# Optimization experiments

Measured on AMD Instinct MI355X. Metric: run time of the kernel, lower is better.

The kernel has to match this reference:

```python
import jax, jax.numpy as jnp
import numpy as np

N_E = 1024
E_DIM = 64


def setup_inputs() -> dict:
    key = jax.random.key(0)
    k_z, k_emb = jax.random.split(key)
    z = jax.random.normal(k_z, (8, 16, 32, 32, E_DIM), dtype=jnp.float32)
    embeddings = jax.random.normal(k_emb, (N_E, E_DIM), dtype=jnp.float32) * 0.02
    return {"z": z, "embeddings": embeddings}


def reference(z, embeddings):
    # flatten all leading dims: [B*T*H*W, e_dim]
    zf = z.reshape(-1, z.shape[-1])
    # squared L2 distance: ||z||^2 + ||e||^2 - 2 z.e  -> [tokens, n_e]
    d = (jnp.sum(zf ** 2, axis=1, keepdims=True)
         + jnp.sum(embeddings ** 2, axis=1)[None, :]
         - 2.0 * jnp.einsum('bd,nd->bn', zf, embeddings))
    idx = jnp.argmin(d, axis=1)
    z_q = embeddings[idx].reshape(z.shape)
    idx = idx.reshape(z.shape[:-1])
    return z_q, idx
```

## Files before the change

kernel.cpp:

```cpp
#include <hip/hip_runtime.h>

typedef short short8 __attribute__((ext_vector_type(8)));
typedef float f32x4 __attribute__((ext_vector_type(4)));

#define NTOK (8 * 16 * 32 * 32)
#define NE 1024
#define ED 64
#define TPB 256
#define MBLK 256
#define NMF 4
#define WKEY (1 << 18)
#define SCALE (-131072.0f)

__device__ __forceinline__ unsigned short bf16_rtne(float f) {
    unsigned u = __float_as_uint(f);
    return (unsigned short)((u + 0x7FFFu + ((u >> 16) & 1u)) >> 16);
}
__device__ __forceinline__ float bf16_to_f32(unsigned short h) {
    return __uint_as_float(((unsigned)h) << 16);
}

__device__ float exact_dist(const float* __restrict__ z, const float* __restrict__ emb,
                            int t, int e) {
    const float* zt = z + (size_t)t * ED;
    const float* ep = emb + (size_t)e * ED;
    float r0 = 0.f, r1 = 0.f, r2 = 0.f, r3 = 0.f;
    float r4 = 0.f, r5 = 0.f, r6 = 0.f, r7 = 0.f;
    for (int d = 0; d < ED; d += 8) {
        r0 += zt[d + 0] * zt[d + 0];
        r1 += zt[d + 1] * zt[d + 1];
        r2 += zt[d + 2] * zt[d + 2];
        r3 += zt[d + 3] * zt[d + 3];
        r4 += zt[d + 4] * zt[d + 4];
        r5 += zt[d + 5] * zt[d + 5];
        r6 += zt[d + 6] * zt[d + 6];
        r7 += zt[d + 7] * zt[d + 7];
    }
    float s1 = ((r0 + r1) + (r2 + r3)) + ((r4 + r5) + (r6 + r7));
    float q0 = 0.f, q1 = 0.f, q2 = 0.f, q3 = 0.f;
    float q4 = 0.f, q5 = 0.f, q6 = 0.f, q7 = 0.f;
    for (int d = 0; d < ED; d += 8) {
        float v0 = ep[d + 0], v1 = ep[d + 1], v2 = ep[d + 2], v3 = ep[d + 3];
        float v4 = ep[d + 4], v5 = ep[d + 5], v6 = ep[d + 6], v7 = ep[d + 7];
        q0 += v0 * v0; q1 += v1 * v1; q2 += v2 * v2; q3 += v3 * v3;
        q4 += v4 * v4; q5 += v5 * v5; q6 += v6 * v6; q7 += v7 * v7;
    }
    float s2 = ((q0 + q1) + (q2 + q3)) + ((q4 + q5) + (q6 + q7));
    float a0 = 0.f, a1 = 0.f, a2 = 0.f, a3 = 0.f;
    for (int d = 0; d < ED; d += 4) {
        a0 = fmaf(zt[d + 0], ep[d + 0], a0);
        a1 = fmaf(zt[d + 1], ep[d + 1], a1);
        a2 = fmaf(zt[d + 2], ep[d + 2], a2);
        a3 = fmaf(zt[d + 3], ep[d + 3], a3);
    }
    float g = (a0 + a1) + (a2 + a3);
    return (s1 + s2) - 2.0f * g;
}

__global__ __launch_bounds__(128) void vq_prep(
    const float* __restrict__ emb,
    unsigned short* __restrict__ bfH,
    unsigned short* __restrict__ bfL,
    float* __restrict__ s2s)
{
    const int f = blockIdx.x * 128 + threadIdx.x;
    const int col = f & 15;
    const int quad = (f >> 4) & 3;
    const int kb = (f >> 6) & 1;
    const int nt = f >> 7;
    const int e = nt * 16 + col;
    const int k0 = kb * 32 + quad * 8;

    const float* p = emb + (size_t)e * ED + k0;
    float4 v0 = *(const float4*)p;
    float4 v1 = *(const float4*)(p + 4);
    float vs[8] = {v0.x, v0.y, v0.z, v0.w, v1.x, v1.y, v1.z, v1.w};
    short8 h, l;
#pragma unroll
    for (int j = 0; j < 8; ++j) {
        float x = vs[j] * SCALE;
        unsigned short hb = bf16_rtne(x);
        float hf = bf16_to_f32(hb);
        unsigned short lb = bf16_rtne(x - hf);
        h[j] = (short)hb;
        l[j] = (short)lb;
    }
    *(short8*)&bfH[(size_t)f * 8] = h;
    *(short8*)&bfL[(size_t)f * 8] = l;

    if (f < 4096) {
        const int row = f >> 2;
        const float4* rp = (const float4*)(emb + (size_t)row * ED + (f & 3) * 16);
        float4 a = rp[0], b = rp[1], c = rp[2], d = rp[3];
        float s = a.x * a.x + a.y * a.y + a.z * a.z + a.w * a.w
                + b.x * b.x + b.y * b.y + b.z * b.z + b.w * b.w
                + c.x * c.x + c.y * c.y + c.z * c.z + c.w * c.w
                + d.x * d.x + d.y * d.y + d.z * d.z + d.w * d.w;
        s += __shfl_xor(s, 1);
        s += __shfl_xor(s, 2);
        if ((f & 3) == 0) s2s[row] = s * 65536.0f;
    }
}

__global__ void __launch_bounds__(TPB) vq_main(
    const float* __restrict__ z,
    const float* __restrict__ emb,
    const unsigned short* __restrict__ bfH,
    const unsigned short* __restrict__ bfL,
    const float* __restrict__ s2s_g,
    float* __restrict__ zq_out,
    float* __restrict__ idx_out)
{
    __shared__ float s2L[NE];
    __shared__ int idx_lds[MBLK];

    const int tid = threadIdx.x;
    const int lane = tid & 63;
    const int wv = __builtin_amdgcn_readfirstlane(tid >> 6);
    const int col = lane & 15;
    const int quad = lane >> 4;
    const int blockTok = blockIdx.x * MBLK;

    for (int i = tid; i < NE; i += TPB) s2L[i] = s2s_g[i];

    short8 Ah[NMF][2], Al[NMF][2];
#pragma unroll
    for (int mf = 0; mf < NMF; ++mf) {
#pragma unroll
        for (int kf = 0; kf < 2; ++kf) {
            const float* zp = z + (size_t)(blockTok + wv * 64 + mf * 16 + col) * ED
                              + kf * 32 + quad * 8;
            float4 v0 = *(const float4*)zp;
            float4 v1 = *(const float4*)(zp + 4);
            float vs[8] = {v0.x, v0.y, v0.z, v0.w, v1.x, v1.y, v1.z, v1.w};
            short8 h, l;
#pragma unroll
            for (int j = 0; j < 8; ++j) {
                float x = vs[j];
                unsigned short hb = bf16_rtne(x);
                float hf = bf16_to_f32(hb);
                unsigned short lb = bf16_rtne(x - hf);
                h[j] = (short)hb;
                l[j] = (short)lb;
            }
            Ah[mf][kf] = h;
            Al[mf][kf] = l;
        }
    }

    int aK[NMF][4], bK[NMF][4];
#pragma unroll
    for (int mf = 0; mf < NMF; ++mf)
#pragma unroll
        for (int r = 0; r < 4; ++r) { aK[mf][r] = 0x7FFFFFFF; bK[mf][r] = 0x7FFFFFFF; }

    const uint4* u4H = (const uint4*)bfH;
    const uint4* u4L = (const uint4*)bfL;

    uint4 cB0 = u4H[lane];
    uint4 cB1 = u4H[64 + lane];
    uint4 cB2 = u4L[lane];
    uint4 cB3 = u4L[64 + lane];

    __syncthreads();

    for (int nt = 0; nt < 64; ++nt) {
        const int nb = (((nt + 1) & 63) << 7) + lane;
        uint4 nB0 = u4H[nb];
        uint4 nB1 = u4H[nb + 64];
        uint4 nB2 = u4L[nb];
        uint4 nB3 = u4L[nb + 64];

        short8 Bh0 = __builtin_bit_cast(short8, cB0);
        short8 Bh1 = __builtin_bit_cast(short8, cB1);
        short8 Bl0 = __builtin_bit_cast(short8, cB2);
        short8 Bl1 = __builtin_bit_cast(short8, cB3);

        const float s2v = s2L[nt * 16 + col];
        const int e = nt * 16 + col;
#pragma unroll
        for (int mf = 0; mf < NMF; ++mf) {
            f32x4 cc = {s2v, s2v, s2v, s2v};
            cc = __builtin_amdgcn_mfma_f32_16x16x32_bf16(Ah[mf][0], Bh0, cc, 0, 0, 0);
            cc = __builtin_amdgcn_mfma_f32_16x16x32_bf16(Ah[mf][1], Bh1, cc, 0, 0, 0);
            cc = __builtin_amdgcn_mfma_f32_16x16x32_bf16(Al[mf][0], Bh0, cc, 0, 0, 0);
            cc = __builtin_amdgcn_mfma_f32_16x16x32_bf16(Al[mf][1], Bh1, cc, 0, 0, 0);
            cc = __builtin_amdgcn_mfma_f32_16x16x32_bf16(Ah[mf][0], Bl0, cc, 0, 0, 0);
            cc = __builtin_amdgcn_mfma_f32_16x16x32_bf16(Ah[mf][1], Bl1, cc, 0, 0, 0);
#pragma unroll
            for (int r = 0; r < 4; ++r) {
                int key = ((int)cc[r]) * 1024 + e;
                const int a0 = aK[mf][r];
                int t1 = min(a0, key);
                int med;
                asm("v_med3_i32 %0, %1, %2, %3"
                    : "=v"(med) : "v"(a0), "v"(bK[mf][r]), "v"(key));
                bK[mf][r] = med;
                aK[mf][r] = t1;
            }
        }

        cB0 = nB0; cB1 = nB1; cB2 = nB2; cB3 = nB3;
    }

#pragma unroll
    for (int mf = 0; mf < NMF; ++mf) {
#pragma unroll
        for (int r = 0; r < 4; ++r) {
            const int a0 = aK[mf][r], b0 = bK[mf][r];
            int A = a0, B = b0;
#pragma unroll
            for (int off = 1; off < 16; off <<= 1) {
                int A2 = __shfl_xor(A, off);
                int B2 = __shfl_xor(B, off);
                int lo = min(A, A2), hi = max(A, A2);
                B = min(min(B, B2), hi);
                A = lo;
            }
            int winner = A & 1023;
            if (B - A <= WKEY) {
                const int t = blockTok + wv * 64 + mf * 16 + quad * 4 + r;
                float dbest = 3.4e38f;
                int ibest = 1 << 30;
                if (a0 <= A + WKEY) {
                    int e = a0 & 1023;
                    float d = exact_dist(z, emb, t, e);
                    if (d < dbest || (d == dbest && e < ibest)) { dbest = d; ibest = e; }
                }
                if (b0 <= A + WKEY) {
                    int e = b0 & 1023;
                    float d = exact_dist(z, emb, t, e);
                    if (d < dbest || (d == dbest && e < ibest)) { dbest = d; ibest = e; }
                }
#pragma unroll
                for (int off = 1; off < 16; off <<= 1) {
                    float d2 = __shfl_xor(dbest, off);
                    int i2 = __shfl_xor(ibest, off);
                    if (d2 < dbest || (d2 == dbest && i2 < ibest)) { dbest = d2; ibest = i2; }
                }
                winner = ibest;
            }
            if (col == 0) idx_lds[wv * 64 + mf * 16 + quad * 4 + r] = winner;
        }
    }

    __syncthreads();

    idx_out[blockTok + tid] = (float)idx_lds[tid];
    const float4* emb_f4 = (const float4*)emb;
    float4* zq_f4 = (float4*)zq_out;
#pragma unroll
    for (int i = 0; i < MBLK * 16 / TPB; ++i) {
        int item = tid + i * TPB;
        int tl = item >> 4, f4 = item & 15;
        int wi = idx_lds[tl];
        zq_f4[(size_t)(blockTok + tl) * 16 + f4] = emb_f4[(size_t)wi * 16 + f4];
    }
}

extern "C" void kernel_launch(void* const* d_in, const int* in_sizes, int n_in,
                              void* d_out, int out_size, void* d_ws, size_t ws_size,
                              hipStream_t stream) {
    const float* z = (const float*)d_in[0];
    const float* emb = (const float*)d_in[1];
    float* out = (float*)d_out;
    float* zq = out;
    float* idx = out + (size_t)NTOK * ED;

    char* ws = (char*)d_ws;
    float* s2s = (float*)ws;
    unsigned short* bfH = (unsigned short*)(ws + 4096);
    unsigned short* bfL = (unsigned short*)(ws + 4096 + 131072);

    vq_prep<<<64, 128, 0, stream>>>(emb, bfH, bfL, s2s);
    vq_main<<<NTOK / MBLK, TPB, 0, stream>>>(z, emb, bfH, bfL, s2s, zq, idx);
}
```

Baseline: 140.1 us.

## Split codebook scan across wave pairs and merge top-2 keys via LDS

Halves tokens per block and assigns two waves to each 64-token group, each scanning half of the codebook (32 of 64 tiles). Partial top-2 keys from the second half are merged through shared memory before the cross-lane reduction and exact-distance refinement. This doubles the block count and shortens each wave's serial MFMA loop, so more waves are in flight and the grid fills the device better. The cost is an extra barrier, an LDS exchange, the A fragments being converted twice per token group, and a refinement phase where half the waves sit idle.

```diff
diff --git a/kernel.cpp b/kernel.cpp
--- a/kernel.cpp
+++ b/kernel.cpp
@@ -7,7 +7,7 @@
 #define NE 1024
 #define ED 64
 #define TPB 256
-#define MBLK 256
+#define MBLK 128
 #define NMF 4
 #define WKEY (1 << 18)
 #define SCALE (-131072.0f)
@@ -113,13 +113,18 @@
 {
     __shared__ float s2L[NE];
     __shared__ int idx_lds[MBLK];
+    __shared__ int mA[2][NMF * 4][64];
+    __shared__ int mB[2][NMF * 4][64];
 
     const int tid = threadIdx.x;
     const int lane = tid & 63;
     const int wv = __builtin_amdgcn_readfirstlane(tid >> 6);
+    const int grp = wv & 1;
+    const int half = wv >> 1;
     const int col = lane & 15;
     const int quad = lane >> 4;
     const int blockTok = blockIdx.x * MBLK;
+    const int tokBase = blockTok + grp * 64;
 
     for (int i = tid; i < NE; i += TPB) s2L[i] = s2s_g[i];
 
@@ -128,7 +133,7 @@
     for (int mf = 0; mf < NMF; ++mf) {
 #pragma unroll
         for (int kf = 0; kf < 2; ++kf) {
-            const float* zp = z + (size_t)(blockTok + wv * 64 + mf * 16 + col) * ED
+            const float* zp = z + (size_t)(tokBase + mf * 16 + col) * ED
                               + kf * 32 + quad * 8;
             float4 v0 = *(const float4*)zp;
             float4 v1 = *(const float4*)(zp + 4);
@@ -157,15 +162,17 @@
     const uint4* u4H = (const uint4*)bfH;
     const uint4* u4L = (const uint4*)bfL;
 
-    uint4 cB0 = u4H[lane];
-    uint4 cB1 = u4H[64 + lane];
-    uint4 cB2 = u4L[lane];
-    uint4 cB3 = u4L[64 + lane];
+    const int sBase = half * 32;
+    uint4 cB0 = u4H[(sBase << 7) + lane];
+    uint4 cB1 = u4H[(sBase << 7) + 64 + lane];
+    uint4 cB2 = u4L[(sBase << 7) + lane];
+    uint4 cB3 = u4L[(sBase << 7) + 64 + lane];
 
     __syncthreads();
 
-    for (int nt = 0; nt < 64; ++nt) {
-        const int nb = (((nt + 1) & 63) << 7) + lane;
+    for (int it = 0; it < 32; ++it) {
+        const int nt = sBase + it;
+        const int nb = ((sBase + ((it + 1) & 31)) << 7) + lane;
         uint4 nB0 = u4H[nb];
         uint4 nB1 = u4H[nb + 64];
         uint4 nB2 = u4L[nb];
@@ -203,50 +210,74 @@
         cB0 = nB0; cB1 = nB1; cB2 = nB2; cB3 = nB3;
     }
 
-#pragma unroll
-    for (int mf = 0; mf < NMF; ++mf) {
-#pragma unroll
-        for (int r = 0; r < 4; ++r) {
-            const int a0 = aK[mf][r], b0 = bK[mf][r];
-            int A = a0, B = b0;
-#pragma unroll
-            for (int off = 1; off < 16; off <<= 1) {
-                int A2 = __shfl_xor(A, off);
-                int B2 = __shfl_xor(B, off);
-                int lo = min(A, A2), hi = max(A, A2);
-                B = min(min(B, B2), hi);
-                A = lo;
-            }
-            int winner = A & 1023;
-            if (B - A <= WKEY) {
-                const int t = blockTok + wv * 64 + mf * 16 + quad * 4 + r;
-                float dbest = 3.4e38f;
-                int ibest = 1 << 30;
-                if (a0 <= A + WKEY) {
-                    int e = a0 & 1023;
-                    float d = exact_dist(z, emb, t, e);
-                    if (d < dbest || (d == dbest && e < ibest)) { dbest = d; ibest = e; }
+    if (half == 1) {
+#pragma unroll
+        for (int mf = 0; mf < NMF; ++mf)
+#pragma unroll
+            for (int r = 0; r < 4; ++r) {
+                mA[grp][mf * 4 + r][lane] = aK[mf][r];
+                mB[grp][mf * 4 + r][lane] = bK[mf][r];
+            }
+    }
+    __syncthreads();
+
+    if (half == 0) {
+#pragma unroll
+        for (int mf = 0; mf < NMF; ++mf)
+#pragma unroll
+            for (int r = 0; r < 4; ++r) {
+                const int a2 = mA[grp][mf * 4 + r][lane];
+                const int b2 = mB[grp][mf * 4 + r][lane];
+                const int a1 = aK[mf][r], b1 = bK[mf][r];
+                aK[mf][r] = min(a1, a2);
+                bK[mf][r] = min(max(a1, a2), min(b1, b2));
+            }
+
+#pragma unroll
+        for (int mf = 0; mf < NMF; ++mf) {
+#pragma unroll
+            for (int r = 0; r < 4; ++r) {
+                const int a0 = aK[mf][r], b0 = bK[mf][r];
+                int A = a0, B = b0;
+#pragma unroll
+                for (int off = 1; off < 16; off <<= 1) {
+                    int A2 = __shfl_xor(A, off);
+                    int B2 = __shfl_xor(B, off);
+                    int lo = min(A, A2), hi = max(A, A2);
+                    B = min(min(B, B2), hi);
+                    A = lo;
                 }
-                if (b0 <= A + WKEY) {
-                    int e = b0 & 1023;
-                    float d = exact_dist(z, emb, t, e);
-                    if (d < dbest || (d == dbest && e < ibest)) { dbest = d; ibest = e; }
+                int winner = A & 1023;
+                if (B - A <= WKEY) {
+                    const int t = tokBase + mf * 16 + quad * 4 + r;
+                    float dbest = 3.4e38f;
+                    int ibest = 1 << 30;
+                    if (a0 <= A + WKEY) {
+                        int e = a0 & 1023;
+                        float d = exact_dist(z, emb, t, e);
+                        if (d < dbest || (d == dbest && e < ibest)) { dbest = d; ibest = e; }
+                    }
+                    if (b0 <= A + WKEY) {
+                        int e = b0 & 1023;
+                        float d = exact_dist(z, emb, t, e);
+                        if (d < dbest || (d == dbest && e < ibest)) { dbest = d; ibest = e; }
+                    }
+#pragma unroll
+                    for (int off = 1; off < 16; off <<= 1) {
+                        float d2 = __shfl_xor(dbest, off);
+                        int i2 = __shfl_xor(ibest, off);
+                        if (d2 < dbest || (d2 == dbest && i2 < ibest)) { dbest = d2; ibest = i2; }
+                    }
+                    winner = ibest;
                 }
-#pragma unroll
-                for (int off = 1; off < 16; off <<= 1) {
-                    float d2 = __shfl_xor(dbest, off);
-                    int i2 = __shfl_xor(ibest, off);
-                    if (d2 < dbest || (d2 == dbest && i2 < ibest)) { dbest = d2; ibest = i2; }
-                }
-                winner = ibest;
-            }
-            if (col == 0) idx_lds[wv * 64 + mf * 16 + quad * 4 + r] = winner;
+                if (col == 0) idx_lds[grp * 64 + mf * 16 + quad * 4 + r] = winner;
+            }
         }
     }
 
     __syncthreads();
 
-    idx_out[blockTok + tid] = (float)idx_lds[tid];
+    if (tid < MBLK) idx_out[blockTok + tid] = (float)idx_lds[tid];
     const float4* emb_f4 = (const float4*)emb;
     float4* zq_f4 = (float4*)zq_out;
 #pragma unroll
```

After: 147.9 us. 5.6% more time.
